# Performance work log

Measured on AMD Instinct MI355X. Metric: run time of the kernel, lower is better.

## Reference

```python
import jax, jax.numpy as jnp
import numpy as np

R = 16
ALPHA = 1
SCALING = ALPHA / R
IN_M, IN_N = 64, 64    # factorization(4096)
OUT_L, OUT_K = 64, 64  # factorization(4096)


def setup_inputs() -> dict:
    key = jax.random.key(0)
    k_x, k1a, k1b, k2a, k2b = jax.random.split(key, 5)
    x = jax.random.normal(k_x, (8192, 4096), dtype=jnp.float32)
    # lokr_w1_a: (r, out_l), lokr_w1_b: (in_m, r), lokr_w2_a: (r, out_k), lokr_w2_b: (in_n, r)
    # (init_weights zeros w1_a; we use random values so the test exercises real math)
    s = 0.05
    w1_a = jax.random.normal(k1a, (R, OUT_L), dtype=jnp.float32) * s
    w1_b = jax.random.normal(k1b, (IN_M, R), dtype=jnp.float32) * s
    w2_a = jax.random.normal(k2a, (R, OUT_K), dtype=jnp.float32) * s
    w2_b = jax.random.normal(k2b, (IN_N, R), dtype=jnp.float32) * s
    return {"x": x, "w1_a": w1_a, "w1_b": w1_b, "w2_a": w2_a, "w2_b": w2_b}


def reference(x, w1_a, w1_b, w2_a, w2_b):
    # w1 = w1_a^T @ w1_b^T -> (out_l, in_m); w2 = w2_a^T @ w2_b^T -> (out_k, in_n)
    w1 = w1_a.T @ w1_b.T
    w2 = w2_a.T @ w2_b.T
    # kron(w1^T, w2^T): (in_m*in_n, out_l*out_k) = (in_features, out_features)
    W = jnp.kron(w1.T, w2.T)
    # dropout rate is 0.0 -> identity
    return (x @ W) * SCALING
```

## Files before the change

kernel.cpp:

```cpp
#include <hip/hip_runtime.h>


typedef __fp16 h2 __attribute__((ext_vector_type(2)));
typedef __fp16 h4 __attribute__((ext_vector_type(4)));
typedef float  f4 __attribute__((ext_vector_type(4)));

__device__ __forceinline__ h4 pack4(float a, float b, float c, float d) {
    h2 lo = __builtin_amdgcn_cvt_pkrtz(a, b);
    h2 hi = __builtin_amdgcn_cvt_pkrtz(c, d);
    h4 r;
    r[0] = lo[0]; r[1] = lo[1]; r[2] = hi[0]; r[3] = hi[1];
    return r;
}

#define MFMA16(a, b, c) __builtin_amdgcn_mfma_f32_16x16x16f16((a), (b), (c), 0, 0, 0)

__global__ __launch_bounds__(256) void lokr_kernel(
    const float* __restrict__ x,
    const float* __restrict__ w1_a,
    const float* __restrict__ w1_b,
    const float* __restrict__ w2_a,
    const float* __restrict__ w2_b,
    float* __restrict__ out)
{
    const int lane = threadIdx.x & 63;
    const int g    = lane >> 4;
    const int c    = lane & 15;
    const int gw   = blockIdx.x * 4 + (threadIdx.x >> 6);
    const size_t b0 = (size_t)gw * 2;

    h4 W2B[4], W1BT[4], W1A[4], W2A[4];
#pragma unroll
    for (int t = 0; t < 4; ++t) {
        const int kb = t * 16 + g * 4;
        W2B[t]  = pack4(w2_b[(kb+0)*16 + c], w2_b[(kb+1)*16 + c],
                        w2_b[(kb+2)*16 + c], w2_b[(kb+3)*16 + c]);
        W1BT[t] = pack4(w1_b[(kb+0)*16 + c], w1_b[(kb+1)*16 + c],
                        w1_b[(kb+2)*16 + c], w1_b[(kb+3)*16 + c]);
        W1A[t]  = pack4(w1_a[(g*4+0)*64 + t*16 + c] * 0.0625f,
                        w1_a[(g*4+1)*64 + t*16 + c] * 0.0625f,
                        w1_a[(g*4+2)*64 + t*16 + c] * 0.0625f,
                        w1_a[(g*4+3)*64 + t*16 + c] * 0.0625f);
        W2A[t]  = pack4(w2_a[(g*4+0)*64 + t*16 + c], w2_a[(g*4+1)*64 + t*16 + c],
                        w2_a[(g*4+2)*64 + t*16 + c], w2_a[(g*4+3)*64 + t*16 + c]);
    }

    const f4 zero = {0.f, 0.f, 0.f, 0.f};

    const float* xp0 = x + b0 * 4096;
    const float* xp1 = xp0 + 4096;
    const int xoff = c * 64 + g * 4;

    auto compute_store = [&](const h4* XA, float* opb) {
        f4 D1[4];
#pragma unroll
        for (int mt = 0; mt < 4; ++mt) {
            f4 a = zero;
#pragma unroll
            for (int nk = 0; nk < 4; ++nk)
                a = MFMA16(XA[mt * 4 + nk], W2B[nk], a);
            D1[mt] = a;
        }
        f4 d2 = zero;
#pragma unroll
        for (int mt = 0; mt < 4; ++mt)
            d2 = MFMA16(W1BT[mt], pack4(D1[mt][0], D1[mt][1], D1[mt][2], D1[mt][3]), d2);
        h4 D2H = pack4(d2[0], d2[1], d2[2], d2[3]);
        h4 D3H[4];
#pragma unroll
        for (int lt = 0; lt < 4; ++lt) {
            f4 d3 = MFMA16(D2H, W1A[lt], zero);
            D3H[lt] = pack4(d3[0], d3[1], d3[2], d3[3]);
        }
        float* op = opb + g * 256 + c;
#pragma unroll
        for (int lt = 0; lt < 4; ++lt) {
#pragma unroll
            for (int kt = 0; kt < 4; ++kt) {
                f4 y = MFMA16(D3H[lt], W2A[kt], zero);
#pragma unroll
                for (int reg = 0; reg < 4; ++reg)
                    op[lt * 1024 + reg * 64 + kt * 16] = y[reg];
            }
        }
    };

    f4 xf[16];
    h4 XA[16];

#pragma unroll
    for (int mt = 0; mt < 4; ++mt)
#pragma unroll
        for (int nk = 0; nk < 4; ++nk)
            xf[mt * 4 + nk] = *(const f4*)&xp0[mt * 1024 + nk * 16 + xoff];
#pragma unroll
    for (int i = 0; i < 16; ++i)
        XA[i] = pack4(xf[i][0], xf[i][1], xf[i][2], xf[i][3]);
#pragma unroll
    for (int mt = 0; mt < 4; ++mt)
#pragma unroll
        for (int nk = 0; nk < 4; ++nk)
            xf[mt * 4 + nk] = *(const f4*)&xp1[mt * 1024 + nk * 16 + xoff];
    __builtin_amdgcn_sched_barrier(0);

    compute_store(XA, out + b0 * 4096);

#pragma unroll
    for (int i = 0; i < 16; ++i)
        XA[i] = pack4(xf[i][0], xf[i][1], xf[i][2], xf[i][3]);
    compute_store(XA, out + (b0 + 1) * 4096);
}

extern "C" void kernel_launch(void* const* d_in, const int* in_sizes, int n_in,
                              void* d_out, int out_size, void* d_ws, size_t ws_size,
                              hipStream_t stream) {
    const float* x    = (const float*)d_in[0];
    const float* w1_a = (const float*)d_in[1];
    const float* w1_b = (const float*)d_in[2];
    const float* w2_a = (const float*)d_in[3];
    const float* w2_b = (const float*)d_in[4];
    float* out = (float*)d_out;

    dim3 grid(1024), block(256);
    hipLaunchKernelGGL(lokr_kernel, grid, block, 0, stream,
                       x, w1_a, w1_b, w2_a, w2_b, out);
}
```

Before: 49.00 us.

## Process four rows per wave with prefetch pipeline and vectorized nontemporal stores

Each wave now handles four rows instead of two, with a loop that loads the next row's x while computing the current one, and the grid is halved to match. The final MFMA swaps its operands so each lane holds four contiguous output floats, which are written as one 16-byte nontemporal store instead of four scalar strided stores. The aim is wider, coalesced writes that bypass the cache and fewer waves amortizing the weight setup. The cost is lower parallelism, with fewer waves available to hide memory latency.

```diff
diff --git a/kernel.cpp b/kernel.cpp
--- a/kernel.cpp
+++ b/kernel.cpp
@@ -15,6 +15,8 @@
 
 #define MFMA16(a, b, c) __builtin_amdgcn_mfma_f32_16x16x16f16((a), (b), (c), 0, 0, 0)
 
+#define ROWS 4
+
 __global__ __launch_bounds__(256) void lokr_kernel(
     const float* __restrict__ x,
     const float* __restrict__ w1_a,
@@ -27,7 +29,7 @@
     const int g    = lane >> 4;
     const int c    = lane & 15;
     const int gw   = blockIdx.x * 4 + (threadIdx.x >> 6);
-    const size_t b0 = (size_t)gw * 2;
+    const size_t b0 = (size_t)gw * ROWS;
 
     h4 W2B[4], W1BT[4], W1A[4], W2A[4];
 #pragma unroll
@@ -46,12 +48,34 @@
     }
 
     const f4 zero = {0.f, 0.f, 0.f, 0.f};
-
-    const float* xp0 = x + b0 * 4096;
-    const float* xp1 = xp0 + 4096;
+    const float* xp = x + b0 * 4096;
     const int xoff = c * 64 + g * 4;
 
-    auto compute_store = [&](const h4* XA, float* opb) {
+    f4 xf[16];
+    h4 XA[16];
+
+#pragma unroll
+    for (int mt = 0; mt < 4; ++mt)
+#pragma unroll
+        for (int nk = 0; nk < 4; ++nk)
+            xf[mt * 4 + nk] = *(const f4*)&xp[mt * 1024 + nk * 16 + xoff];
+
+#pragma unroll
+    for (int rr = 0; rr < ROWS; ++rr) {
+#pragma unroll
+        for (int i = 0; i < 16; ++i)
+            XA[i] = pack4(xf[i][0], xf[i][1], xf[i][2], xf[i][3]);
+
+        if (rr + 1 < ROWS) {
+#pragma unroll
+            for (int mt = 0; mt < 4; ++mt)
+#pragma unroll
+                for (int nk = 0; nk < 4; ++nk)
+                    xf[mt * 4 + nk] = *(const f4*)&xp[(size_t)(rr + 1) * 4096 +
+                                                     mt * 1024 + nk * 16 + xoff];
+        }
+        __builtin_amdgcn_sched_barrier(0);
+
         f4 D1[4];
 #pragma unroll
         for (int mt = 0; mt < 4; ++mt) {
@@ -72,43 +96,17 @@
             f4 d3 = MFMA16(D2H, W1A[lt], zero);
             D3H[lt] = pack4(d3[0], d3[1], d3[2], d3[3]);
         }
-        float* op = opb + g * 256 + c;
+        float* op = out + (b0 + rr) * 4096;
 #pragma unroll
         for (int lt = 0; lt < 4; ++lt) {
 #pragma unroll
             for (int kt = 0; kt < 4; ++kt) {
-                f4 y = MFMA16(D3H[lt], W2A[kt], zero);
-#pragma unroll
-                for (int reg = 0; reg < 4; ++reg)
-                    op[lt * 1024 + reg * 64 + kt * 16] = y[reg];
+                f4 y = MFMA16(W2A[kt], D3H[lt], zero);
+                __builtin_nontemporal_store(
+                    y, reinterpret_cast<f4*>(op + (lt * 16 + c) * 64 + kt * 16 + g * 4));
             }
         }
-    };
-
-    f4 xf[16];
-    h4 XA[16];
-
-#pragma unroll
-    for (int mt = 0; mt < 4; ++mt)
-#pragma unroll
-        for (int nk = 0; nk < 4; ++nk)
-            xf[mt * 4 + nk] = *(const f4*)&xp0[mt * 1024 + nk * 16 + xoff];
-#pragma unroll
-    for (int i = 0; i < 16; ++i)
-        XA[i] = pack4(xf[i][0], xf[i][1], xf[i][2], xf[i][3]);
-#pragma unroll
-    for (int mt = 0; mt < 4; ++mt)
-#pragma unroll
-        for (int nk = 0; nk < 4; ++nk)
-            xf[mt * 4 + nk] = *(const f4*)&xp1[mt * 1024 + nk * 16 + xoff];
-    __builtin_amdgcn_sched_barrier(0);
-
-    compute_store(XA, out + b0 * 4096);
-
-#pragma unroll
-    for (int i = 0; i < 16; ++i)
-        XA[i] = pack4(xf[i][0], xf[i][1], xf[i][2], xf[i][3]);
-    compute_store(XA, out + (b0 + 1) * 4096);
+    }
 }
 
 extern "C" void kernel_launch(void* const* d_in, const int* in_sizes, int n_in,
@@ -121,7 +119,7 @@
     const float* w2_b = (const float*)d_in[4];
     float* out = (float*)d_out;
 
-    dim3 grid(1024), block(256);
+    dim3 grid(512), block(256);
     hipLaunchKernelGGL(lokr_kernel, grid, block, 0, stream,
                        x, w1_a, w1_b, w2_a, w2_b, out);
 }
```

Result: slower. 58.88 us (+20.1%).
